# Kernel optimization log

Hardware: AMD Instinct MI355X
Metric: run time of the kernel (lower is better)

The kernel has to match this reference:

```python
import jax, jax.numpy as jnp
import numpy as np
from jax import lax

B_SZ, SEQ, D_MODEL, D_STATE, DT_RANK = 4, 4096, 256, 16, 16


def setup_inputs() -> dict:
    key = jax.random.key(0)
    ks = jax.random.split(key, 12)
    d, n, r = D_MODEL, D_STATE, DT_RANK
    inp = {}
    inp["hidden_states"] = jax.random.normal(ks[0], (B_SZ, SEQ, d), jnp.float32)
    inp["in_proj_w"] = jax.random.normal(ks[1], (3 * d, d), jnp.float32) * (d ** -0.5)
    inp["x_proj_w"] = jax.random.normal(ks[2], (r + 2 * n, d), jnp.float32) * (d ** -0.5)
    s = r ** -0.5
    inp["dt_proj_w"] = jax.random.uniform(ks[3], (d, r), jnp.float32, -s, s)
    dt = jnp.exp(jax.random.uniform(ks[4], (d,), jnp.float32) * (np.log(0.1) - np.log(1e-3)) + np.log(1e-3))
    inp["dt_proj_b"] = dt + jnp.log(-jnp.expm1(-dt))  # inverse-softplus init
    inp["A_log"] = jnp.log(jnp.broadcast_to(jnp.arange(1, n + 1, dtype=jnp.float32), (d, n)))
    inp["D"] = jnp.ones((d,), jnp.float32)
    inp["out_proj1_w"] = jax.random.normal(ks[5], (d, d), jnp.float32) * (d ** -0.5)
    inp["conv_x_w"] = jax.random.normal(ks[6], (d, 1, 1), jnp.float32)
    inp["conv_x_b"] = jax.random.normal(ks[7], (d,), jnp.float32) * 0.1
    inp["conv_y_w"] = jax.random.normal(ks[8], (d, 1, 3), jnp.float32) * (3 ** -0.5)
    inp["conv_y_b"] = jax.random.normal(ks[9], (d,), jnp.float32) * 0.1
    inp["conv_z_w"] = jax.random.normal(ks[10], (d, 1, 5), jnp.float32) * (5 ** -0.5)
    inp["conv_z_b"] = jax.random.normal(ks[11], (d,), jnp.float32) * 0.1
    return inp


def _silu(x):
    return x * jax.nn.sigmoid(x)


def _dwconv(x, w, b):
    # x: (b, d, l); w: (d, 1, k) depthwise; 'same' padding (odd k)
    k = w.shape[-1]
    pad = (k - 1) // 2
    out = lax.conv_general_dilated(
        x, w, window_strides=(1,), padding=[(pad, pad)],
        dimension_numbers=("NCH", "OIH", "NCH"), feature_group_count=x.shape[1])
    return out + b[None, :, None]


def _selective_scan(u, delta, A, B, C, D, delta_bias):
    # u, delta: (b,d,l); A: (d,n); B,C: (b,n,l); D, delta_bias: (d,)
    delta = jax.nn.softplus(delta + delta_bias[None, :, None])
    dA = jnp.exp(jnp.einsum("bdl,dn->lbdn", delta, A))          # (l,b,d,n)
    dBu = jnp.einsum("bdl,bnl,bdl->lbdn", delta, B, u)           # (l,b,d,n)
    Ct = jnp.transpose(C, (2, 0, 1))                             # (l,b,n)

    def step(h, inp):
        dA_t, dBu_t, C_t = inp
        h = dA_t * h + dBu_t                                     # (b,d,n)
        y = jnp.einsum("bdn,bn->bd", h, C_t)
        return h, y

    h0 = jnp.zeros(u.shape[:2] + (A.shape[1],), u.dtype)
    _, ys = lax.scan(step, h0, (dA, dBu, Ct))                    # ys: (l,b,d)
    y = jnp.transpose(ys, (1, 2, 0))                             # (b,d,l)
    return y + D[None, :, None] * u


def reference(hidden_states, in_proj_w, x_proj_w, dt_proj_w, dt_proj_b, A_log, D,
              out_proj1_w, conv_x_w, conv_x_b, conv_y_w, conv_y_b, conv_z_w, conv_z_b):
    b, l, d = hidden_states.shape
    xyz = jnp.einsum("ble,de->bdl", hidden_states, in_proj_w)    # (b, 3d, l)
    x, y, z = jnp.split(xyz, 3, axis=1)                          # each (b,d,l)
    A = -jnp.exp(A_log.astype(jnp.float32))
    x = _silu(_dwconv(x, conv_x_w, conv_x_b))
    y = _silu(_dwconv(y, conv_y_w, conv_y_b))
    z = _silu(_dwconv(z, conv_z_w, conv_z_b))
    x_dbl = jnp.einsum("bdl,ed->ble", x, x_proj_w)               # (b,l,r+2n)
    dt_r, Bm, Cm = jnp.split(x_dbl, [DT_RANK, DT_RANK + D_STATE], axis=-1)
    # dt_proj applies bias here; selective_scan adds delta_bias again (faithful to source)
    dt = jnp.einsum("blr,dr->bdl", dt_r, dt_proj_w) + dt_proj_b[None, :, None]
    Bm = jnp.transpose(Bm, (0, 2, 1))                            # (b,n,l)
    Cm = jnp.transpose(Cm, (0, 2, 1))
    p = _selective_scan(x, dt, A, Bm, Cm, D.astype(jnp.float32), dt_proj_b.astype(jnp.float32))
    p = jnp.transpose(p, (0, 2, 1))                              # (b,l,d)
    y = jnp.transpose(y, (0, 2, 1))
    z = jnp.transpose(z, (0, 2, 1))
    l1 = jnp.einsum("bld,ed->ble", p * y, out_proj1_w)
    l2 = l1 * z
    l2 = _dwconv(jnp.transpose(l2, (0, 2, 1)), conv_x_w, conv_x_b)
    return jnp.transpose(l2, (0, 2, 1))                          # (b,l,d)
```

## Files before the change

kernel.cpp:

```cpp
#include <hip/hip_runtime.h>
#include <hip/hip_bf16.h>
#include <math.h>

typedef __hip_bfloat16 bf16;
typedef __attribute__((ext_vector_type(8))) short bf16x8;
typedef __attribute__((ext_vector_type(4))) float f32x4;

#define B_SZ 4
#define SEQ  4096
#define DM   256
#define NST  16
#define NCHK 64
#define LC   (SEQ/NCHK)
#define MT   (B_SZ*SEQ)
#define NLIN (B_SZ*16*256)

#define LOG2E 1.4426950408889634f

__device__ __forceinline__ float silu_f(float v){ return v / (1.f + __expf(-v)); }
__device__ __forceinline__ float softplus_f(float v){
  return (v > 15.f) ? v : __logf(1.f + __expf(v));
}
__device__ __forceinline__ short f2bf(float f){
  union { bf16 h; short s; } u; u.h = __float2bfloat16(f); return u.s;
}
__device__ __forceinline__ float bf2f(short s){
  union { unsigned int i; float f; } v;
  v.i = ((unsigned int)(unsigned short)s) << 16; return v.f;
}
__device__ __forceinline__ unsigned short f2h(float f){
  union { unsigned short u; _Float16 h; } v; v.h = (_Float16)f; return v.u;
}
__device__ __forceinline__ float h2f(unsigned short s){
  union { unsigned short u; _Float16 h; } v; v.u = s; return (float)v.h;
}
__device__ __forceinline__ short4 f4_to_bf4(float4 f){
  short4 s; s.x = f2bf(f.x); s.y = f2bf(f.y); s.z = f2bf(f.z); s.w = f2bf(f.w);
  return s;
}
__device__ __forceinline__ bf16x8 f8_to_bf8(float4 a, float4 b){
  bf16x8 v;
  v[0]=f2bf(a.x); v[1]=f2bf(a.y); v[2]=f2bf(a.z); v[3]=f2bf(a.w);
  v[4]=f2bf(b.x); v[5]=f2bf(b.y); v[6]=f2bf(b.z); v[7]=f2bf(b.w);
  return v;
}

__device__ __forceinline__ void async_cp16(const short* g, short* l){
  __builtin_amdgcn_global_load_lds(
      (const __attribute__((address_space(1))) unsigned int*)g,
      (__attribute__((address_space(3))) unsigned int*)l, 16, 0, 0);
}

template<int CTRL>
__device__ __forceinline__ float dpp_add_step(float v){
  int x = __builtin_amdgcn_update_dpp(0, __float_as_int(v), CTRL, 0xf, 0xf, true);
  return v + __int_as_float(x);
}

__global__ __launch_bounds__(256)
void cvt_w_k(const float* __restrict__ w_in, const float* __restrict__ w_o1,
             short* __restrict__ w_in_b, short* __restrict__ w_o1_b)
{
  int i = blockIdx.x * 256 + threadIdx.x;
  if (i < 49152) {
    float4 q = *(const float4*)&w_in[i * 4];
    *(short4*)&w_in_b[i * 4] = f4_to_bf4(q);
  } else {
    int j = i - 49152;
    float4 q = *(const float4*)&w_o1[j * 4];
    *(short4*)&w_o1_b[j * 4] = f4_to_bf4(q);
  }
}

__global__ __launch_bounds__(256)
void mfma_gemm_conv_k(const float* __restrict__ Av,
                      const short* __restrict__ Bw,
                      const float* __restrict__ wx, const float* __restrict__ bx,
                      const float* __restrict__ wy, const float* __restrict__ by,
                      const float* __restrict__ wz, const float* __restrict__ bz,
                      short* __restrict__ xout, short* __restrict__ yout,
                      short* __restrict__ zout)
{
  constexpr int RM = 80;
  __shared__ __align__(16) char smem_c[26624];
  short* As = (short*)smem_c;
  short* Bs = (short*)(smem_c + 10240);
  const int tid  = threadIdx.x;
  const int wave = tid >> 6, lane = tid & 63;
  const int quad = lane >> 4, l16 = lane & 15;
  const int wn = wave * 32;
  const int m0 = blockIdx.x * 64, n0 = blockIdx.y * 128;

  f32x4 acc[5][2] = {};

  for (int k0 = 0; k0 < 256; k0 += 64) {
    #pragma unroll
    for (int p = 0; p < 4; p++) {
      int id = p * 256 + tid;
      int row = id >> 3, slot = id & 7;
      int gch = slot ^ (row & 7);
      async_cp16(Bw + (size_t)(n0 + row) * 256 + k0 + gch * 8,
                 &Bs[row * 64 + slot * 8]);
    }
    #pragma unroll
    for (int p = 0; p < 3; p++) {
      int id = p * 256 + tid;
      if (id < RM * 8) {
        int row = id >> 3, slot = id & 7;
        int gch = slot ^ (row & 7);
        int gm = m0 - 8 + row;
        gm = gm < 0 ? 0 : (gm > MT - 1 ? MT - 1 : gm);
        const float* src = Av + (size_t)gm * 256 + k0 + gch * 8;
        float4 q0 = *(const float4*)src;
        float4 q1 = *(const float4*)(src + 4);
        *(bf16x8*)&As[row * 64 + slot * 8] = f8_to_bf8(q0, q1);
      }
    }
    __syncthreads();
    #pragma unroll
    for (int ks = 0; ks < 2; ks++) {
      bf16x8 fa[5], fb[2];
      int sa = (ks * 4 + quad) ^ (l16 & 7);
      #pragma unroll
      for (int i = 0; i < 5; i++)
        fa[i] = *(const bf16x8*)&As[(i * 16 + l16) * 64 + sa * 8];
      #pragma unroll
      for (int j = 0; j < 2; j++)
        fb[j] = *(const bf16x8*)&Bs[(wn + j * 16 + l16) * 64 + sa * 8];
      #pragma unroll
      for (int i = 0; i < 5; i++)
        #pragma unroll
        for (int j = 0; j < 2; j++)
          acc[i][j] = __builtin_amdgcn_mfma_f32_16x16x32_bf16(fa[i], fb[j], acc[i][j], 0, 0, 0);
    }
    __syncthreads();
  }

  short* Ts = (short*)smem_c;
  #pragma unroll
  for (int i = 0; i < 5; i++) {
    #pragma unroll
    for (int j = 0; j < 2; j++) {
      int col = wn + j * 16 + l16;
      int row = i * 16 + quad * 4;
      short4 v;
      v.x = f2bf(acc[i][j][0]); v.y = f2bf(acc[i][j][1]);
      v.z = f2bf(acc[i][j][2]); v.w = f2bf(acc[i][j][3]);
      *(short4*)&Ts[col * 84 + row] = v;
    }
  }
  __syncthreads();

  const int cp = tid & 63, rg = tid >> 6;
  const int lc0 = cp * 2;
  const int lr0 = rg * 16;
  const int lbase = (m0 & (SEQ - 1)) + lr0;
  float ta[24], tb[24];
  {
    const short* q0 = &Ts[lc0 * 84 + lr0 + 4];
    #pragma unroll
    for (int q = 0; q < 6; q++) {
      short4 a = *(const short4*)&q0[q * 4];
      short4 b = *(const short4*)&q0[84 + q * 4];
      ta[q*4+0] = bf2f(a.x); ta[q*4+1] = bf2f(a.y);
      ta[q*4+2] = bf2f(a.z); ta[q*4+3] = bf2f(a.w);
      tb[q*4+0] = bf2f(b.x); tb[q*4+1] = bf2f(b.y);
      tb[q*4+2] = bf2f(b.z); tb[q*4+3] = bf2f(b.w);
    }
  }
  const int type = n0 >> 8;
  const int gq = n0 + lc0 - type * 256;
  if (type == 0) {
    float w0 = wx[gq], w1 = wx[gq + 1];
    float b0 = bx[gq], b1 = bx[gq + 1];
    #pragma unroll
    for (int t = 0; t < 16; t++) {
      short2 o;
      o.x = f2bf(silu_f(fmaf(ta[t + 4], w0, b0)));
      o.y = f2bf(silu_f(fmaf(tb[t + 4], w1, b1)));
      *(short2*)&xout[(size_t)(m0 + lr0 + t) * 256 + gq] = o;
    }
  } else if (type == 1) {
    float w0[3], w1[3];
    #pragma unroll
    for (int j = 0; j < 3; j++) { w0[j] = wy[gq*3 + j]; w1[j] = wy[(gq+1)*3 + j]; }
    float b0 = by[gq], b1 = by[gq + 1];
    #pragma unroll
    for (int t = 0; t < 16; t++) {
      float a0 = b0, a1 = b1;
      #pragma unroll
      for (int j = 0; j < 3; j++) {
        int l = lbase + t + j - 1;
        bool ok = ((unsigned)l < SEQ);
        a0 = fmaf(ok ? ta[t + 3 + j] : 0.f, w0[j], a0);
        a1 = fmaf(ok ? tb[t + 3 + j] : 0.f, w1[j], a1);
      }
      short2 o; o.x = f2bf(silu_f(a0)); o.y = f2bf(silu_f(a1));
      *(short2*)&yout[(size_t)(m0 + lr0 + t) * 256 + gq] = o;
    }
  } else {
    float w0[5], w1[5];
    #pragma unroll
    for (int j = 0; j < 5; j++) { w0[j] = wz[gq*5 + j]; w1[j] = wz[(gq+1)*5 + j]; }
    float b0 = bz[gq], b1 = bz[gq + 1];
    #pragma unroll
    for (int t = 0; t < 16; t++) {
      float a0 = b0, a1 = b1;
      #pragma unroll
      for (int j = 0; j < 5; j++) {
        int l = lbase + t + j - 2;
        bool ok = ((unsigned)l < SEQ);
        a0 = fmaf(ok ? ta[t + 2 + j] : 0.f, w0[j], a0);
        a1 = fmaf(ok ? tb[t + 2 + j] : 0.f, w1[j], a1);
      }
      short2 o; o.x = f2bf(silu_f(a0)); o.y = f2bf(silu_f(a1));
      *(short2*)&zout[(size_t)(m0 + lr0 + t) * 256 + gq] = o;
    }
  }
}

template<int EPI, bool OBF, int BM>
__global__ __launch_bounds__(256)
void mfma_gemm_k(const short* __restrict__ Av, const short* __restrict__ Bw,
                 void* __restrict__ Outv, int N, int K,
                 const float* __restrict__ bias, const short* __restrict__ zc,
                 const float* __restrict__ cwx)
{
  constexpr int BN = 128, BK = 64;
  constexpr int JF = (BM == 64) ? 2 : 4;
  __shared__ short As[BM * BK];
  __shared__ short Bs[BN * BK];
  const int tid  = threadIdx.x;
  const int wave = tid >> 6, lane = tid & 63;
  const int quad = lane >> 4, l16 = lane & 15;
  const int wm = (BM == 64) ? 0 : (wave & 1) * 64;
  const int wn = (BM == 64) ? wave * 32 : (wave >> 1) * 64;
  const int m0 = blockIdx.x * BM, n0 = blockIdx.y * BN;

  f32x4 acc[4][JF] = {};

  for (int k0 = 0; k0 < K; k0 += BK) {
    #pragma unroll
    for (int p = 0; p < BM * 8 / 256; p++) {
      int id = p * 256 + tid;
      int row = id >> 3, slot = id & 7;
      int gch = slot ^ (row & 7);
      async_cp16(Av + (size_t)(m0 + row) * K + k0 + gch * 8,
                 &As[row * 64 + slot * 8]);
    }
    #pragma unroll
    for (int p = 0; p < 4; p++) {
      int id = p * 256 + tid;
      int row = id >> 3, slot = id & 7;
      int gch = slot ^ (row & 7);
      async_cp16(Bw + (size_t)(n0 + row) * K + k0 + gch * 8,
                 &Bs[row * 64 + slot * 8]);
    }
    __syncthreads();
    #pragma unroll
    for (int ks = 0; ks < 2; ks++) {
      bf16x8 fa[4], fb[JF];
      int sa = (ks * 4 + quad) ^ (l16 & 7);
      #pragma unroll
      for (int i = 0; i < 4; i++)
        fa[i] = *(const bf16x8*)&As[(wm + i * 16 + l16) * 64 + sa * 8];
      #pragma unroll
      for (int j = 0; j < JF; j++)
        fb[j] = *(const bf16x8*)&Bs[(wn + j * 16 + l16) * 64 + sa * 8];
      #pragma unroll
      for (int i = 0; i < 4; i++)
        #pragma unroll
        for (int j = 0; j < JF; j++)
          acc[i][j] = __builtin_amdgcn_mfma_f32_16x16x32_bf16(fa[i], fb[j], acc[i][j], 0, 0, 0);
    }
    __syncthreads();
  }

  #pragma unroll
  for (int i = 0; i < 4; i++) {
    #pragma unroll
    for (int j = 0; j < JF; j++) {
      int n = n0 + wn + j * 16 + l16;
      #pragma unroll
      for (int r = 0; r < 4; r++) {
        int m = m0 + wm + i * 16 + quad * 4 + r;
        float v = acc[i][j][r];
        if constexpr (EPI == 2)
          v = v * bf2f(zc[(size_t)m * N + n]) * cwx[n] + bias[n];
        if constexpr (OBF) ((short*)Outv)[(size_t)m * N + n] = f2bf(v);
        else               ((float*)Outv)[(size_t)m * N + n] = v;
      }
    }
  }
}

__global__ __launch_bounds__(256)
void gemm34_k(const short* __restrict__ xcb,
              const float* __restrict__ Bw,
              const float* __restrict__ wdt,
              const float* __restrict__ bdt,
              float* __restrict__ xdbl,
              unsigned short* __restrict__ dtvh)
{
  constexpr int TM = 32, TK = 16, NN = 48;
  __shared__ __align__(16) float As[TK][TM + 4];
  __shared__ __align__(16) float Bs[TK][64 + 4];
  __shared__ __align__(16) float dt_s[TM][20];
  __shared__ __align__(16) float wdt_s[256][20];
  const int tid = threadIdx.x;
  const int tn = tid & 15, tm = tid >> 4;
  const int m0 = blockIdx.x * TM;
  float acc[2][4] = {};
  const int mlA = tid >> 3, kdA = (tid & 7) * 2;
  const int mlB = tid >> 2, kqB = (tid & 3) * 4;

  {
    float4 q0 = *(const float4*)&wdt[tid * 16 + 0];
    float4 q1 = *(const float4*)&wdt[tid * 16 + 4];
    float4 q2 = *(const float4*)&wdt[tid * 16 + 8];
    float4 q3 = *(const float4*)&wdt[tid * 16 + 12];
    *(float4*)&wdt_s[tid][0]  = q0;
    *(float4*)&wdt_s[tid][4]  = q1;
    *(float4*)&wdt_s[tid][8]  = q2;
    *(float4*)&wdt_s[tid][12] = q3;
  }

  for (int k0 = 0; k0 < 256; k0 += TK) {
    {
      size_t off = (size_t)(m0 + mlA) * 256 + k0 + kdA;
      unsigned int v = *(const unsigned int*)(xcb + off);
      As[kdA + 0][mlA] = bf2f((short)(v & 0xffffu));
      As[kdA + 1][mlA] = bf2f((short)(v >> 16));
    }
    {
      float v0 = 0.f, v1 = 0.f, v2 = 0.f, v3 = 0.f;
      if (mlB < NN) {
        float4 q = *(const float4*)(Bw + (size_t)mlB * 256 + k0 + kqB);
        v0 = q.x; v1 = q.y; v2 = q.z; v3 = q.w;
      }
      Bs[kqB+0][mlB] = v0; Bs[kqB+1][mlB] = v1; Bs[kqB+2][mlB] = v2; Bs[kqB+3][mlB] = v3;
    }
    __syncthreads();
    #pragma unroll
    for (int k = 0; k < TK; k++) {
      float2 av = *(const float2*)&As[k][tm << 1];
      float4 bv = *(const float4*)&Bs[k][tn << 2];
      float a[2] = {av.x, av.y};
      float b[4] = {bv.x, bv.y, bv.z, bv.w};
      #pragma unroll
      for (int i = 0; i < 2; i++)
        #pragma unroll
        for (int j = 0; j < 4; j++)
          acc[i][j] = fmaf(a[i], b[j], acc[i][j]);
    }
    __syncthreads();
  }

  #pragma unroll
  for (int i = 0; i < 2; i++) {
    int m = m0 + (tm << 1) + i;
    #pragma unroll
    for (int j = 0; j < 4; j++) {
      int n = (tn << 2) + j;
      float v = acc[i][j];
      if (n < NN) xdbl[(size_t)m * NN + n] = v;
      if (tn < 4) dt_s[(tm << 1) + i][n] = v;
    }
  }
  __syncthreads();

  const int c0 = tid & 63, rg = tid >> 6;
  float w[4][16];
  float bb[4];
  #pragma unroll
  for (int cc = 0; cc < 4; cc++) {
    int col = cc * 64 + c0;
    #pragma unroll
    for (int q = 0; q < 4; q++) {
      float4 t = *(const float4*)&wdt_s[col][q * 4];
      w[cc][q*4+0] = t.x; w[cc][q*4+1] = t.y; w[cc][q*4+2] = t.z; w[cc][q*4+3] = t.w;
    }
    bb[cc] = 2.f * bdt[col];
  }
  #pragma unroll
  for (int rr = 0; rr < 8; rr++) {
    int row = rg * 8 + rr;
    float dr[16];
    #pragma unroll
    for (int q = 0; q < 4; q++) {
      float4 t = *(const float4*)&dt_s[row][q * 4];
      dr[q*4+0] = t.x; dr[q*4+1] = t.y; dr[q*4+2] = t.z; dr[q*4+3] = t.w;
    }
    #pragma unroll
    for (int cc = 0; cc < 4; cc++) {
      float s = bb[cc];
      #pragma unroll
      for (int k = 0; k < 16; k++) s = fmaf(dr[k], w[cc][k], s);
      dtvh[(size_t)(m0 + row) * 256 + cc * 64 + c0] = f2h(softplus_f(s));
    }
  }
}

__global__ __launch_bounds__(256)
void scan_a_k(const short* __restrict__ xcb,
              const unsigned short* __restrict__ dtvh,
              const float* __restrict__ xdbl,
              const float* __restrict__ A_log,
              float* __restrict__ Sdt, float* __restrict__ hfbuf)
{
  __shared__ __align__(16) float2 du2_s[16 * 66];
  __shared__ __align__(16) float  Bc_s [16 * 68];
  const int tid = threadIdx.x;
  const int n = tid & 15, dl = tid >> 4;
  const int ch = blockIdx.x;
  const int d0 = blockIdx.y * 16;
  const int b  = blockIdx.z;
  const int d  = d0 + dl;
  const int t0 = ch * LC;
  const size_t brow = (size_t)b * SEQ;
  const size_t cidx = (size_t)ch * NLIN + ((size_t)b * 16 + blockIdx.y) * 256 + tid;

  {
    const int tq = tid >> 2;
    const int dq = (tid & 3) * 4;
    size_t row = brow + t0 + tq;
    ushort4 xv = *(const ushort4*)(xcb + row * 256 + d0 + dq);
    ushort4 dv = *(const ushort4*)(dtvh + row * 256 + d0 + dq);
    float dt0 = h2f(dv.x), dt1 = h2f(dv.y), dt2 = h2f(dv.z), dt3 = h2f(dv.w);
    du2_s[(dq + 0) * 66 + tq] = make_float2(dt0, dt0 * bf2f((short)xv.x));
    du2_s[(dq + 1) * 66 + tq] = make_float2(dt1, dt1 * bf2f((short)xv.y));
    du2_s[(dq + 2) * 66 + tq] = make_float2(dt2, dt2 * bf2f((short)xv.z));
    du2_s[(dq + 3) * 66 + tq] = make_float2(dt3, dt3 * bf2f((short)xv.w));
    float4 Bq = *(const float4*)(xdbl + row * 48 + 16 + dq);
    Bc_s[(dq + 0) * 68 + tq] = Bq.x;
    Bc_s[(dq + 1) * 68 + tq] = Bq.y;
    Bc_s[(dq + 2) * 68 + tq] = Bq.z;
    Bc_s[(dq + 3) * 68 + tq] = Bq.w;
  }
  __syncthreads();

  const float A2 = -__expf(A_log[d * NST + n]) * LOG2E;

  float S = 0.f;
  for (int t4 = 0; t4 < LC; t4 += 4) {
    float4 a = *(const float4*)&du2_s[dl * 66 + t4];
    float4 c = *(const float4*)&du2_s[dl * 66 + t4 + 2];
    S += (a.x + a.z) + (c.x + c.z);
  }

  float r = S;
  float ac0 = 0.f, ac1 = 0.f, ac2 = 0.f, ac3 = 0.f;
  for (int t4 = 0; t4 < LC; t4 += 4) {
    float4 a = *(const float4*)&du2_s[dl * 66 + t4];
    float4 c = *(const float4*)&du2_s[dl * 66 + t4 + 2];
    float r0 = r - a.x;
    float r1 = r0 - a.z;
    float r2 = r1 - c.x;
    float r3 = r2 - c.z;
    r = r3;
    float4 f = *(const float4*)&Bc_s[n * 68 + t4];
    ac0 = fmaf(a.y * f.x, __builtin_amdgcn_exp2f(A2 * r0), ac0);
    ac1 = fmaf(a.w * f.y, __builtin_amdgcn_exp2f(A2 * r1), ac1);
    ac2 = fmaf(c.y * f.z, __builtin_amdgcn_exp2f(A2 * r2), ac2);
    ac3 = fmaf(c.w * f.w, __builtin_amdgcn_exp2f(A2 * r3), ac3);
  }

  hfbuf[cidx] = (ac0 + ac1) + (ac2 + ac3);
  if (n == 0)
    Sdt[((size_t)ch * B_SZ + b) * 256 + d] = S;
}

__global__ __launch_bounds__(64)
void scan_mid_k(const float* __restrict__ Sdt, const float* __restrict__ hfbuf,
                const float* __restrict__ A_log, float* __restrict__ Hstart)
{
  int lin = blockIdx.x * 64 + threadIdx.x;
  int b = lin >> 12;
  int d = (lin >> 4) & 255;
  int n = lin & 15;
  const float A2 = -__expf(A_log[d * NST + n]) * LOG2E;
  float H = 0.f;
  for (int c = 0; c < NCHK; c++) {
    size_t idx = (size_t)c * NLIN + lin;
    Hstart[idx] = H;
    float P = __builtin_amdgcn_exp2f(A2 * Sdt[((size_t)c * B_SZ + b) * 256 + d]);
    H = P * H + hfbuf[idx];
  }
}

__global__ __launch_bounds__(64)
void scan_c_k(const short* __restrict__ xcb,
              const unsigned short* __restrict__ dtvh,
              const float* __restrict__ xdbl,
              const float* __restrict__ A_log,
              const float* __restrict__ Dp,
              const float* __restrict__ Hstart,
              const short* __restrict__ ycb,
              short* __restrict__ poutb)
{
  __shared__ __align__(16) float2 du2_s[16 * 66];
  __shared__ __align__(16) float2 BC_s [64 * 18];
  __shared__ __align__(16) float  y_s  [16 * 68];
  const int tid = threadIdx.x;
  const int ch = blockIdx.x;
  const int d0 = blockIdx.y * 16;
  const int b  = blockIdx.z;
  const int t0 = ch * LC;
  const size_t brow = (size_t)b * SEQ;

  {
    const int r = tid;
    size_t row = brow + t0 + r;
    #pragma unroll
    for (int q = 0; q < 4; q++) {
      ushort4 xv = *(const ushort4*)(xcb + row * 256 + d0 + q * 4);
      ushort4 dv = *(const ushort4*)(dtvh + row * 256 + d0 + q * 4);
      float dt0 = h2f(dv.x), dt1 = h2f(dv.y), dt2 = h2f(dv.z), dt3 = h2f(dv.w);
      du2_s[(q*4 + 0) * 66 + r] = make_float2(dt0, dt0 * bf2f((short)xv.x));
      du2_s[(q*4 + 1) * 66 + r] = make_float2(dt1, dt1 * bf2f((short)xv.y));
      du2_s[(q*4 + 2) * 66 + r] = make_float2(dt2, dt2 * bf2f((short)xv.z));
      du2_s[(q*4 + 3) * 66 + r] = make_float2(dt3, dt3 * bf2f((short)xv.w));
    }
    #pragma unroll
    for (int q = 0; q < 4; q++) {
      float4 Bq = *(const float4*)(xdbl + row * 48 + 16 + q * 4);
      float4 Cq = *(const float4*)(xdbl + row * 48 + 32 + q * 4);
      *(float4*)&BC_s[r * 18 + q * 4 + 0] = make_float4(Bq.x, Cq.x, Bq.y, Cq.y);
      *(float4*)&BC_s[r * 18 + q * 4 + 2] = make_float4(Bq.z, Cq.z, Bq.w, Cq.w);
    }
  }
  __syncthreads();

  const int dl = tid >> 2, nq = tid & 3;
  const int d  = d0 + dl;

  float A2[4], h[4];
  #pragma unroll
  for (int j = 0; j < 4; j++)
    A2[j] = -__expf(A_log[d * NST + nq * 4 + j]) * LOG2E;
  {
    const size_t cb = (size_t)ch * NLIN +
                      ((size_t)b * 16 + blockIdx.y) * 256 + dl * 16 + nq * 4;
    float4 H = *(const float4*)(Hstart + cb);
    h[0] = H.x; h[1] = H.y; h[2] = H.z; h[3] = H.w;
  }

  for (int t4 = 0; t4 < LC; t4 += 4) {
    float4 a = *(const float4*)&du2_s[dl * 66 + t4];
    float4 c = *(const float4*)&du2_s[dl * 66 + t4 + 2];
    float dts[4] = {a.x, a.z, c.x, c.z};
    float dus[4] = {a.y, a.w, c.y, c.w};
    float yv[4];
    #pragma unroll
    for (int tt = 0; tt < 4; tt++) {
      float4 e = *(const float4*)&BC_s[(t4 + tt) * 18 + nq * 4];
      float4 g = *(const float4*)&BC_s[(t4 + tt) * 18 + nq * 4 + 2];
      float dA0 = __builtin_amdgcn_exp2f(dts[tt] * A2[0]);
      float dA1 = __builtin_amdgcn_exp2f(dts[tt] * A2[1]);
      float dA2 = __builtin_amdgcn_exp2f(dts[tt] * A2[2]);
      float dA3 = __builtin_amdgcn_exp2f(dts[tt] * A2[3]);
      h[0] = fmaf(dA0, h[0], dus[tt] * e.x);
      h[1] = fmaf(dA1, h[1], dus[tt] * e.z);
      h[2] = fmaf(dA2, h[2], dus[tt] * g.x);
      h[3] = fmaf(dA3, h[3], dus[tt] * g.z);
      float s = h[0] * e.y;
      s = fmaf(h[1], e.w, s);
      s = fmaf(h[2], g.y, s);
      s = fmaf(h[3], g.w, s);
      yv[tt] = s;
    }
    #pragma unroll
    for (int j = 0; j < 4; j++) yv[j] = dpp_add_step<0x112>(yv[j]);
    #pragma unroll
    for (int j = 0; j < 4; j++) yv[j] = dpp_add_step<0x111>(yv[j]);
    if (nq == 3)
      *(float4*)&y_s[dl * 68 + t4] = make_float4(yv[0], yv[1], yv[2], yv[3]);
  }
  __syncthreads();

  {
    const int r = tid;
    size_t row = brow + t0 + r;
    #pragma unroll
    for (int q = 0; q < 4; q++) {
      ushort4 xv = *(const ushort4*)(xcb + row * 256 + d0 + q * 4);
      ushort4 yg = *(const ushort4*)(ycb + row * 256 + d0 + q * 4);
      short4 o;
      float p0 = fmaf(Dp[d0 + q*4 + 0], bf2f((short)xv.x), y_s[(q*4 + 0) * 68 + r]);
      float p1 = fmaf(Dp[d0 + q*4 + 1], bf2f((short)xv.y), y_s[(q*4 + 1) * 68 + r]);
      float p2 = fmaf(Dp[d0 + q*4 + 2], bf2f((short)xv.z), y_s[(q*4 + 2) * 68 + r]);
      float p3 = fmaf(Dp[d0 + q*4 + 3], bf2f((short)xv.w), y_s[(q*4 + 3) * 68 + r]);
      o.x = f2bf(p0 * bf2f((short)yg.x));
      o.y = f2bf(p1 * bf2f((short)yg.y));
      o.z = f2bf(p2 * bf2f((short)yg.z));
      o.w = f2bf(p3 * bf2f((short)yg.w));
      *(short4*)&poutb[row * 256 + d0 + q * 4] = o;
    }
  }
}

extern "C" void kernel_launch(void* const* d_in, const int* in_sizes, int n_in,
                              void* d_out, int out_size, void* d_ws, size_t ws_size,
                              hipStream_t stream)
{
  const float* hs    = (const float*)d_in[0];
  const float* w_in  = (const float*)d_in[1];
  const float* w_xp  = (const float*)d_in[2];
  const float* w_dt  = (const float*)d_in[3];
  const float* b_dt  = (const float*)d_in[4];
  const float* A_log = (const float*)d_in[5];
  const float* Dp    = (const float*)d_in[6];
  const float* w_o1  = (const float*)d_in[7];
  const float* cwx   = (const float*)d_in[8];
  const float* cbx   = (const float*)d_in[9];
  const float* cwy   = (const float*)d_in[10];
  const float* cby   = (const float*)d_in[11];
  const float* cwz   = (const float*)d_in[12];
  const float* cbz   = (const float*)d_in[13];

  char* wsb = (char*)d_ws;
  short* xcb  = (short*)wsb;
  short* ycb  = xcb + (size_t)MT * 256;
  short* zcb  = ycb + (size_t)MT * 256;
  short* pbufb= zcb + (size_t)MT * 256;
  short* w_in_b = pbufb + (size_t)MT * 256;
  short* w_o1_b = w_in_b + 768 * 256;
  float* xdbl = (float*)(w_o1_b + 256 * 256 + 128);
  unsigned short* dtvh = (unsigned short*)(xdbl + (size_t)MT * 48);
  float* Sdtb = (float*)(dtvh + (size_t)MT * 256);
  float* hf   = Sdtb + (size_t)NCHK * B_SZ * 256;
  float* Hs   = hf   + (size_t)NCHK * NLIN;

  dim3 blk(256);

  cvt_w_k<<<dim3(256), blk, 0, stream>>>(w_in, w_o1, w_in_b, w_o1_b);

  mfma_gemm_conv_k<<<dim3(MT / 64, 768 / 128), blk, 0, stream>>>(
      hs, w_in_b, cwx, cbx, cwy, cby, cwz, cbz, xcb, ycb, zcb);

  gemm34_k<<<dim3(MT / 32), blk, 0, stream>>>(
      xcb, w_xp, w_dt, b_dt, xdbl, dtvh);

  scan_a_k<<<dim3(NCHK, DM / 16, B_SZ), blk, 0, stream>>>(
      xcb, dtvh, xdbl, A_log, Sdtb, hf);
  scan_mid_k<<<dim3(NLIN / 64), dim3(64), 0, stream>>>(Sdtb, hf, A_log, Hs);
  scan_c_k<<<dim3(NCHK, DM / 16, B_SZ), dim3(64), 0, stream>>>(
      xcb, dtvh, xdbl, A_log, Dp, Hs, ycb, pbufb);

  mfma_gemm_k<2, false, 128><<<dim3(MT / 128, 256 / 128), blk, 0, stream>>>(
      pbufb, w_o1_b, d_out, 256, 256, cbx, zcb, cwx);
}
```

Measured before the change: 195.3 us.

## Move x_proj GEMM to bf16 MFMA with hi/lo weight split and reorder grid

```diff
diff --git a/kernel.cpp b/kernel.cpp
--- a/kernel.cpp
+++ b/kernel.cpp
@@ -59,16 +59,27 @@
 
 __global__ __launch_bounds__(256)
 void cvt_w_k(const float* __restrict__ w_in, const float* __restrict__ w_o1,
-             short* __restrict__ w_in_b, short* __restrict__ w_o1_b)
+             const float* __restrict__ w_xp,
+             short* __restrict__ w_in_b, short* __restrict__ w_o1_b,
+             short* __restrict__ wxp_hi, short* __restrict__ wxp_lo)
 {
   int i = blockIdx.x * 256 + threadIdx.x;
   if (i < 49152) {
     float4 q = *(const float4*)&w_in[i * 4];
     *(short4*)&w_in_b[i * 4] = f4_to_bf4(q);
-  } else {
+  } else if (i < 65536) {
     int j = i - 49152;
     float4 q = *(const float4*)&w_o1[j * 4];
     *(short4*)&w_o1_b[j * 4] = f4_to_bf4(q);
+  } else {
+    int j = i - 65536;
+    float4 q = *(const float4*)&w_xp[j * 4];
+    short4 h = f4_to_bf4(q);
+    *(short4*)&wxp_hi[j * 4] = h;
+    float4 r;
+    r.x = q.x - bf2f(h.x); r.y = q.y - bf2f(h.y);
+    r.z = q.z - bf2f(h.z); r.w = q.w - bf2f(h.w);
+    *(short4*)&wxp_lo[j * 4] = f4_to_bf4(r);
   }
 }
 
@@ -89,7 +100,7 @@
   const int wave = tid >> 6, lane = tid & 63;
   const int quad = lane >> 4, l16 = lane & 15;
   const int wn = wave * 32;
-  const int m0 = blockIdx.x * 64, n0 = blockIdx.y * 128;
+  const int m0 = blockIdx.y * 64, n0 = blockIdx.x * 128;
 
   f32x4 acc[5][2] = {};
 
@@ -296,23 +307,22 @@
 
 __global__ __launch_bounds__(256)
 void gemm34_k(const short* __restrict__ xcb,
-              const float* __restrict__ Bw,
+              const short* __restrict__ wxp_hi,
+              const short* __restrict__ wxp_lo,
               const float* __restrict__ wdt,
               const float* __restrict__ bdt,
               float* __restrict__ xdbl,
               unsigned short* __restrict__ dtvh)
 {
-  constexpr int TM = 32, TK = 16, NN = 48;
-  __shared__ __align__(16) float As[TK][TM + 4];
-  __shared__ __align__(16) float Bs[TK][64 + 4];
-  __shared__ __align__(16) float dt_s[TM][20];
+  __shared__ __align__(16) short As[64 * 64];
+  __shared__ __align__(16) short Bh[48 * 64];
+  __shared__ __align__(16) short Bl[48 * 64];
+  __shared__ __align__(16) float dt_s[64][20];
   __shared__ __align__(16) float wdt_s[256][20];
   const int tid = threadIdx.x;
-  const int tn = tid & 15, tm = tid >> 4;
-  const int m0 = blockIdx.x * TM;
-  float acc[2][4] = {};
-  const int mlA = tid >> 3, kdA = (tid & 7) * 2;
-  const int mlB = tid >> 2, kqB = (tid & 3) * 4;
+  const int wave = tid >> 6, lane = tid & 63;
+  const int quad = lane >> 4, l16 = lane & 15;
+  const int m0 = blockIdx.x * 64;
 
   {
     float4 q0 = *(const float4*)&wdt[tid * 16 + 0];
@@ -325,46 +335,62 @@
     *(float4*)&wdt_s[tid][12] = q3;
   }
 
-  for (int k0 = 0; k0 < 256; k0 += TK) {
-    {
-      size_t off = (size_t)(m0 + mlA) * 256 + k0 + kdA;
-      unsigned int v = *(const unsigned int*)(xcb + off);
-      As[kdA + 0][mlA] = bf2f((short)(v & 0xffffu));
-      As[kdA + 1][mlA] = bf2f((short)(v >> 16));
-    }
-    {
-      float v0 = 0.f, v1 = 0.f, v2 = 0.f, v3 = 0.f;
-      if (mlB < NN) {
-        float4 q = *(const float4*)(Bw + (size_t)mlB * 256 + k0 + kqB);
-        v0 = q.x; v1 = q.y; v2 = q.z; v3 = q.w;
+  f32x4 acc[3] = {};
+
+  for (int k0 = 0; k0 < 256; k0 += 64) {
+    #pragma unroll
+    for (int p = 0; p < 2; p++) {
+      int id = p * 256 + tid;
+      int row = id >> 3, slot = id & 7;
+      int gch = slot ^ (row & 7);
+      async_cp16(xcb + (size_t)(m0 + row) * 256 + k0 + gch * 8,
+                 &As[row * 64 + slot * 8]);
+    }
+    #pragma unroll
+    for (int p = 0; p < 2; p++) {
+      int id = p * 256 + tid;
+      if (id < 384) {
+        int row = id >> 3, slot = id & 7;
+        int gch = slot ^ (row & 7);
+        async_cp16(wxp_hi + (size_t)row * 256 + k0 + gch * 8,
+                   &Bh[row * 64 + slot * 8]);
       }
-      Bs[kqB+0][mlB] = v0; Bs[kqB+1][mlB] = v1; Bs[kqB+2][mlB] = v2; Bs[kqB+3][mlB] = v3;
+    }
+    #pragma unroll
+    for (int p = 0; p < 2; p++) {
+      int id = p * 256 + tid;
+      if (id < 384) {
+        int row = id >> 3, slot = id & 7;
+        int gch = slot ^ (row & 7);
+        async_cp16(wxp_lo + (size_t)row * 256 + k0 + gch * 8,
+                   &Bl[row * 64 + slot * 8]);
+      }
     }
     __syncthreads();
     #pragma unroll
-    for (int k = 0; k < TK; k++) {
-      float2 av = *(const float2*)&As[k][tm << 1];
-      float4 bv = *(const float4*)&Bs[k][tn << 2];
-      float a[2] = {av.x, av.y};
-      float b[4] = {bv.x, bv.y, bv.z, bv.w};
-      #pragma unroll
-      for (int i = 0; i < 2; i++)
-        #pragma unroll
-        for (int j = 0; j < 4; j++)
-          acc[i][j] = fmaf(a[i], b[j], acc[i][j]);
+    for (int ks = 0; ks < 2; ks++) {
+      int sa = (ks * 4 + quad) ^ (l16 & 7);
+      bf16x8 fa = *(const bf16x8*)&As[(wave * 16 + l16) * 64 + sa * 8];
+      #pragma unroll
+      for (int j = 0; j < 3; j++) {
+        bf16x8 fbh = *(const bf16x8*)&Bh[(j * 16 + l16) * 64 + sa * 8];
+        bf16x8 fbl = *(const bf16x8*)&Bl[(j * 16 + l16) * 64 + sa * 8];
+        acc[j] = __builtin_amdgcn_mfma_f32_16x16x32_bf16(fa, fbh, acc[j], 0, 0, 0);
+        acc[j] = __builtin_amdgcn_mfma_f32_16x16x32_bf16(fa, fbl, acc[j], 0, 0, 0);
+      }
     }
     __syncthreads();
   }
 
   #pragma unroll
-  for (int i = 0; i < 2; i++) {
-    int m = m0 + (tm << 1) + i;
-    #pragma unroll
-    for (int j = 0; j < 4; j++) {
-      int n = (tn << 2) + j;
-      float v = acc[i][j];
-      if (n < NN) xdbl[(size_t)m * NN + n] = v;
-      if (tn < 4) dt_s[(tm << 1) + i][n] = v;
+  for (int j = 0; j < 3; j++) {
+    int n = j * 16 + l16;
+    #pragma unroll
+    for (int r = 0; r < 4; r++) {
+      int mrow = wave * 16 + quad * 4 + r;
+      float v = acc[j][r];
+      xdbl[(size_t)(m0 + mrow) * 48 + n] = v;
+      if (j == 0) dt_s[mrow][n] = v;
     }
   }
   __syncthreads();
@@ -383,8 +409,8 @@
     bb[cc] = 2.f * bdt[col];
   }
   #pragma unroll
-  for (int rr = 0; rr < 8; rr++) {
-    int row = rg * 8 + rr;
+  for (int rr = 0; rr < 16; rr++) {
+    int row = rg * 16 + rr;
     float dr[16];
     #pragma unroll
     for (int q = 0; q < 4; q++) {
@@ -625,7 +651,9 @@
   short* pbufb= zcb + (size_t)MT * 256;
   short* w_in_b = pbufb + (size_t)MT * 256;
   short* w_o1_b = w_in_b + 768 * 256;
-  float* xdbl = (float*)(w_o1_b + 256 * 256 + 128);
+  short* wxp_hi = w_o1_b + 256 * 256;
+  short* wxp_lo = wxp_hi + 48 * 256;
+  float* xdbl = (float*)(wxp_lo + 48 * 256 + 128);
   unsigned short* dtvh = (unsigned short*)(xdbl + (size_t)MT * 48);
   float* Sdtb = (float*)(dtvh + (size_t)MT * 256);
   float* hf   = Sdtb + (size_t)NCHK * B_SZ * 256;
@@ -633,13 +661,14 @@
 
   dim3 blk(256);
 
-  cvt_w_k<<<dim3(256), blk, 0, stream>>>(w_in, w_o1, w_in_b, w_o1_b);
-
-  mfma_gemm_conv_k<<<dim3(MT / 64, 768 / 128), blk, 0, stream>>>(
+  cvt_w_k<<<dim3(268), blk, 0, stream>>>(w_in, w_o1, w_xp,
+                                         w_in_b, w_o1_b, wxp_hi, wxp_lo);
+
+  mfma_gemm_conv_k<<<dim3(768 / 128, MT / 64), blk, 0, stream>>>(
       hs, w_in_b, cwx, cbx, cwy, cby, cwz, cbz, xcb, ycb, zcb);
 
-  gemm34_k<<<dim3(MT / 32), blk, 0, stream>>>(
-      xcb, w_xp, w_dt, b_dt, xdbl, dtvh);
+  gemm34_k<<<dim3(MT / 64), blk, 0, stream>>>(
+      xcb, wxp_hi, wxp_lo, w_dt, b_dt, xdbl, dtvh);
 
   scan_a_k<<<dim3(NCHK, DM / 16, B_SZ), blk, 0, stream>>>(
       xcb, dtvh, xdbl, A_log, Sdtb, hf);
```

New measurement: 192.5 us. About the same (-1.4%).
